# Kernel tuning notes

Measured on AMD Instinct MI355X. Metric: run time of the kernel, lower is better.

The kernel has to match this reference:

```python
import jax, jax.numpy as jnp
import numpy as np

D_MODEL = 2048; D_STATE = 64; D_CONV = 4; EXPAND = 2
N_HEADS = 64; N_GROUPS = 1; CHUNK = 256
D_INNER = D_MODEL * EXPAND            # 4096
HEAD_DIM = D_INNER // N_HEADS         # 64
XBC_DIM = D_INNER + 2 * N_GROUPS * D_STATE   # 4224
D_IN_PROJ = 2 * D_INNER + 2 * N_GROUPS * D_STATE + N_HEADS  # 8384
EPS = 1.1920929e-07  # torch.finfo(float32).eps (nn.RMSNorm default)


def setup_inputs() -> dict:
    key = jax.random.key(0)
    ks = jax.random.split(key, 4)
    x = jax.random.normal(ks[0], (2, 2048, D_MODEL), jnp.float32)
    in_proj_w = jax.random.normal(ks[1], (D_IN_PROJ, D_MODEL), jnp.float32) * (D_MODEL ** -0.5)
    conv_w = jax.random.normal(ks[2], (XBC_DIM, 1, D_CONV), jnp.float32) * (D_CONV ** -0.5)
    conv_b = jnp.zeros((XBC_DIM,), jnp.float32)
    rng = np.random.default_rng(0)
    dt = np.exp(rng.standard_normal(N_HEADS) * (np.log(0.1) - np.log(0.001)) + np.log(0.001))
    dt = np.clip(dt, 1e-4, None)
    dt_bias = jnp.asarray(dt + np.log(-np.expm1(-dt)), jnp.float32)
    A_log = jnp.asarray(np.log(rng.uniform(1.0, 16.0, N_HEADS)), jnp.float32)
    D_param = jnp.ones((N_HEADS,), jnp.float32)
    norm_w = jnp.ones((D_INNER,), jnp.float32)
    out_proj_w = jax.random.normal(ks[3], (D_MODEL, D_INNER), jnp.float32) * (D_INNER ** -0.5)
    return dict(x=x, in_proj_w=in_proj_w, conv_w=conv_w, conv_b=conv_b,
                dt_bias=dt_bias, A_log=A_log, D_param=D_param,
                norm_w=norm_w, out_proj_w=out_proj_w)


def segsum(a):
    # a: (..., T) -> lower-triangular segment sums, -inf above diagonal
    T = a.shape[-1]
    cs = jnp.cumsum(a, axis=-1)
    seg = cs[..., :, None] - cs[..., None, :]
    mask = jnp.tril(jnp.ones((T, T), dtype=bool))
    return jnp.where(mask, seg, -jnp.inf)


def ssd_minimal_discrete(X, A, B, C, block_len):
    # X: (b,l,h,p)  A: (b,l,h)  B,C: (b,l,h,n)
    b, l, h, p = X.shape
    c = l // block_len
    X = X.reshape(b, c, block_len, h, p)
    A = A.reshape(b, c, block_len, h).transpose(0, 3, 1, 2)  # b h c l
    B = B.reshape(b, c, block_len, h, -1)
    C = C.reshape(b, c, block_len, h, -1)
    A_cumsum = jnp.cumsum(A, axis=-1)
    # 1. intra-chunk (diagonal block) output
    L = jnp.exp(segsum(A))
    Y_diag = jnp.einsum('bclhn,bcshn,bhcls,bcshp->bclhp', C, B, L, X)
    # 2. per-chunk states
    decay_states = jnp.exp(A_cumsum[..., -1:] - A_cumsum)
    states = jnp.einsum('bclhn,bhcl,bclhp->bchpn', B, decay_states, X)
    # 3. inter-chunk recurrence (initial state = 0)
    states = jnp.concatenate([jnp.zeros_like(states[:, :1]), states], axis=1)
    decay_chunk = jnp.exp(segsum(jnp.pad(A_cumsum[..., -1], ((0, 0), (0, 0), (1, 0)))))
    new_states = jnp.einsum('bhzc,bchpn->bzhpn', decay_chunk, states)
    states_in, final_state = new_states[:, :-1], new_states[:, -1]
    # 4. state -> output conversion
    Y_off = jnp.einsum('bclhn,bchpn,bhcl->bclhp', C, states_in, jnp.exp(A_cumsum))
    return (Y_diag + Y_off).reshape(b, l, h, p), final_state


def reference(x, in_proj_w, conv_w, conv_b, dt_bias, A_log, D_param, norm_w, out_proj_w):
    b, L, _ = x.shape
    A = -jnp.exp(A_log)                                     # (h,)
    zxbcdt = x @ in_proj_w.T                                # (b,L,d_in_proj)
    z = zxbcdt[..., :D_INNER]
    xBC = zxbcdt[..., D_INNER:D_INNER + XBC_DIM]
    dt = jax.nn.softplus(zxbcdt[..., D_INNER + XBC_DIM:] + dt_bias)  # (b,L,h)
    # causal depthwise conv1d (padding=d_conv-1, then truncate to seqlen)
    xc = jax.lax.conv_general_dilated(
        xBC.transpose(0, 2, 1), conv_w, (1,), [(D_CONV - 1, 0)],
        dimension_numbers=('NCH', 'OIH', 'NCH'), feature_group_count=XBC_DIM)
    xBC = jax.nn.silu(xc + conv_b[None, :, None]).transpose(0, 2, 1)
    xs = xBC[..., :D_INNER].reshape(b, L, N_HEADS, HEAD_DIM)
    Bm = xBC[..., D_INNER:D_INNER + N_GROUPS * D_STATE].reshape(b, L, N_GROUPS, D_STATE)
    Cm = xBC[..., D_INNER + N_GROUPS * D_STATE:].reshape(b, L, N_GROUPS, D_STATE)
    rep = N_HEADS // N_GROUPS
    Bm = jnp.repeat(Bm, rep, axis=2)
    Cm = jnp.repeat(Cm, rep, axis=2)
    y, _ = ssd_minimal_discrete(xs * dt[..., None], A * dt, Bm, Cm, CHUNK)
    y = y + xs * D_param[None, None, :, None]
    y = y.reshape(b, L, D_INNER)
    y = z * jax.nn.silu(y)
    y = y * jax.lax.rsqrt(jnp.mean(y * y, axis=-1, keepdims=True) + EPS) * norm_w
    return y @ out_proj_w.T
```

## Files before the change

### kernel.cpp

```cpp
#include <hip/hip_runtime.h>
#include <math.h>

#define D_MODEL   2048
#define D_INNER   4096
#define XBC_DIM   4224
#define D_IN_PROJ 8384
#define N_ZX      8320
#define NH    64
#define HD    64
#define DS    64
#define LCH   256
#define NCH   8
#define LSEQ  2048
#define TTOK  4096
#define EPS_R 1.1920929e-07f

#define XT_S 264
#define WL_S 72
#define GEMM_IN_BLKS ((N_ZX / 128) * (TTOK / 128))

typedef unsigned short u16;
typedef unsigned int   u32;
typedef _Float16 f16x8 __attribute__((ext_vector_type(8)));
typedef _Float16 f16x4 __attribute__((ext_vector_type(4)));
typedef float    f4v   __attribute__((ext_vector_type(4)));

__device__ __forceinline__ float4 f16_ld4(const _Float16* c, size_t idx) {
    f16x4 v = *(const f16x4*)(c + idx);
    return make_float4((float)v[0], (float)v[1], (float)v[2], (float)v[3]);
}
__device__ __forceinline__ f16x8 cvt8(float4 a, float4 b) {
    f16x8 r;
    r[0] = (_Float16)a.x; r[1] = (_Float16)a.y; r[2] = (_Float16)a.z; r[3] = (_Float16)a.w;
    r[4] = (_Float16)b.x; r[5] = (_Float16)b.y; r[6] = (_Float16)b.z; r[7] = (_Float16)b.w;
    return r;
}
__device__ __forceinline__ float fexp(float x)  { return __expf(x); }
__device__ __forceinline__ float fsilu(float x) { return x / (1.f + __expf(-x)); }
__device__ __forceinline__ int xcd_swz(int orig, int nwg) {
    int cpx = nwg >> 3;
    return (orig & 7) * cpx + (orig >> 3);
}
__device__ __forceinline__ void gload16(const _Float16* g, _Float16* l) {
    __builtin_amdgcn_global_load_lds(
        (const __attribute__((address_space(1))) u32*)g,
        (__attribute__((address_space(3))) u32*)l, 16, 0, 0);
}

#define NX8  ((size_t)TTOK * D_MODEL / 8)
#define NW8  ((size_t)N_ZX * D_MODEL / 8)
#define NO8  ((size_t)D_MODEL * D_INNER / 8)
__global__ __launch_bounds__(256) void cvt_all_kernel(const float* __restrict__ x,
                                                      const float* __restrict__ w_in,
                                                      const float* __restrict__ w_out,
                                                      const float* __restrict__ nw,
                                                      _Float16* __restrict__ x16,
                                                      _Float16* __restrict__ win16,
                                                      _Float16* __restrict__ wout16) {
    size_t i = (size_t)blockIdx.x * 256 + threadIdx.x;
    if (i < NX8) {
        size_t base = i * 8;
        float4 a = *(const float4*)(x + base);
        float4 b = *(const float4*)(x + base + 4);
        *(f16x8*)(x16 + base) = cvt8(a, b);
    } else if (i < NX8 + NW8) {
        size_t base = (i - NX8) * 8;
        float4 a = *(const float4*)(w_in + base);
        float4 b = *(const float4*)(w_in + base + 4);
        *(f16x8*)(win16 + base) = cvt8(a, b);
    } else if (i < NX8 + NW8 + NO8) {
        size_t base = (i - NX8 - NW8) * 8;
        int k = (int)(base & 4095);
        float4 a = *(const float4*)(w_out + base);
        float4 b = *(const float4*)(w_out + base + 4);
        float4 na = *(const float4*)(nw + k);
        float4 nb = *(const float4*)(nw + k + 4);
        a.x *= na.x; a.y *= na.y; a.z *= na.z; a.w *= na.w;
        b.x *= nb.x; b.y *= nb.y; b.z *= nb.z; b.w *= nb.w;
        *(f16x8*)(wout16 + base) = cvt8(a, b);
    }
}

__global__ __launch_bounds__(256) void gemm_in_dt(const _Float16* __restrict__ A,
                                                  const _Float16* __restrict__ W,
                                                  _Float16* __restrict__ zf,
                                                  _Float16* __restrict__ cbuf,
                                                  const float* __restrict__ x,
                                                  const float* __restrict__ w_in,
                                                  const float* __restrict__ dt_bias,
                                                  float* __restrict__ dt_buf) {
    __shared__ __align__(16) char smem[65536];
    const int tid = threadIdx.x;

    if (blockIdx.x < 256) {
        float* Xs = (float*)smem;
        float* Ws = (float*)(smem + 4096);
        int t0 = blockIdx.x * 16;
        int h = tid & 63, trow = tid >> 6;
        float acc[4] = {0.f, 0.f, 0.f, 0.f};
        const float* wdt = w_in + (size_t)(D_INNER + XBC_DIM) * D_MODEL;

        for (int k0 = 0; k0 < D_MODEL; k0 += 64) {
            __syncthreads();
            {
                int r = tid >> 4, c4 = (tid & 15) * 4;
                *(float4*)&Xs[r * 64 + c4] =
                    *(const float4*)(x + (size_t)(t0 + r) * D_MODEL + k0 + c4);
            }
            #pragma unroll
            for (int i = 0; i < 4; ++i) {
                int ff = tid + i * 256;
                int r = ff >> 4, c4 = (ff & 15) * 4;
                float4 v = *(const float4*)(wdt + (size_t)r * D_MODEL + k0 + c4);
                Ws[r * 65 + c4 + 0] = v.x; Ws[r * 65 + c4 + 1] = v.y;
                Ws[r * 65 + c4 + 2] = v.z; Ws[r * 65 + c4 + 3] = v.w;
            }
            __syncthreads();
            #pragma unroll 16
            for (int k = 0; k < 64; ++k) {
                float wv = Ws[h * 65 + k];
                #pragma unroll
                for (int i = 0; i < 4; ++i)
                    acc[i] += Xs[(trow + i * 4) * 64 + k] * wv;
            }
        }
        float bias = dt_bias[h];
        #pragma unroll
        for (int i = 0; i < 4; ++i) {
            float xv = acc[i] + bias;
            float sp = (xv > 20.f) ? xv : log1pf(expf(xv));
            dt_buf[(size_t)(t0 + trow + i * 4) * 64 + h] = sp;
        }
        return;
    }

    _Float16* lsA = (_Float16*)smem;
    _Float16* lsB = (_Float16*)(smem + 32768);
    const int lane = tid & 63, w = tid >> 6;
    int swz = xcd_swz((int)blockIdx.x - 256, GEMM_IN_BLKS);
    const int row0 = (swz / (N_ZX / 128)) * 128, col0 = (swz % (N_ZX / 128)) * 128;
    const int wr = w >> 1, wc = w & 1;
    const int fr = lane & 15, fq = lane >> 4;

    auto stage = [&](int buf, int k0) {
        #pragma unroll
        for (int i = 0; i < 4; ++i) {
            int obase = i * 4096 + w * 1024;
            int o = obase + lane * 16;
            int row = o >> 7, b0 = o & 127;
            int lb = b0 ^ ((row & 7) << 4);
            gload16(A + (size_t)(row0 + row) * D_MODEL + k0 + (lb >> 1),
                    lsA + buf * 8192 + (obase >> 1));
            gload16(W + (size_t)(col0 + row) * D_MODEL + k0 + (lb >> 1),
                    lsB + buf * 8192 + (obase >> 1));
        }
    };

    f4v acc[4][4];
    #pragma unroll
    for (int mi = 0; mi < 4; ++mi)
        #pragma unroll
        for (int ni = 0; ni < 4; ++ni) acc[mi][ni] = (f4v){0.f, 0.f, 0.f, 0.f};

    stage(0, 0);
    __syncthreads();
    int cur = 0;
    for (int k0 = 0; k0 < D_MODEL; k0 += 64) {
        if (k0 + 64 < D_MODEL) stage(cur ^ 1, k0 + 64);
        f16x8 ah[4][2];
        #pragma unroll
        for (int mi = 0; mi < 4; ++mi)
            #pragma unroll
            for (int kf = 0; kf < 2; ++kf) {
                int r = wr * 64 + mi * 16 + fr;
                int pb = (kf * 64 + fq * 16) ^ ((r & 7) << 4);
                ah[mi][kf] = *(const f16x8*)((const char*)lsA + cur * 16384 + r * 128 + pb);
            }
        #pragma unroll
        for (int ni = 0; ni < 4; ++ni) {
            #pragma unroll
            for (int kf = 0; kf < 2; ++kf) {
                int rb = wc * 64 + ni * 16 + fr;
                int pb = (kf * 64 + fq * 16) ^ ((rb & 7) << 4);
                f16x8 bh = *(const f16x8*)((const char*)lsB + cur * 16384 + rb * 128 + pb);
                #pragma unroll
                for (int mi = 0; mi < 4; ++mi)
                    acc[mi][ni] = __builtin_amdgcn_mfma_f32_16x16x32_f16(ah[mi][kf], bh, acc[mi][ni], 0, 0, 0);
            }
        }
        __syncthreads();
        cur ^= 1;
    }

    const int orow = fq * 4;
    #pragma unroll
    for (int mi = 0; mi < 4; ++mi)
        #pragma unroll
        for (int ni = 0; ni < 4; ++ni) {
            int r = row0 + wr * 64 + mi * 16 + orow;
            int cc = col0 + wc * 64 + ni * 16 + fr;
            if (col0 < D_INNER) {
                #pragma unroll
                for (int j = 0; j < 4; ++j)
                    zf[(size_t)(r + j) * D_INNER + cc] = (_Float16)acc[mi][ni][j];
            } else {
                #pragma unroll
                for (int j = 0; j < 4; ++j)
                    cbuf[(size_t)(r + j) * XBC_DIM + (cc - D_INNER)] = (_Float16)acc[mi][ni][j];
            }
        }
}

__global__ __launch_bounds__(256) void scan_bc_kernel(const float* __restrict__ dt_buf,
                                                      const float* __restrict__ A_log,
                                                      float* __restrict__ acs,
                                                      const _Float16* __restrict__ cbuf,
                                                      const float* __restrict__ cw,
                                                      const float* __restrict__ cb,
                                                      _Float16* __restrict__ bc) {
    int tid = threadIdx.x;
    if (blockIdx.x < 1024) {
        int bh = blockIdx.x >> 3, c = blockIdx.x & 7;
        int b = bh >> 6, h = bh & 63;
        float Ah = -expf(A_log[h]);
        __shared__ float s[256];
        int t = b * LSEQ + c * LCH + tid;
        float a = Ah * dt_buf[t * 64 + h];
        s[tid] = a;
        __syncthreads();
        for (int off = 1; off < 256; off <<= 1) {
            float v = (tid >= off) ? s[tid - off] : 0.f;
            __syncthreads();
            s[tid] += v;
            __syncthreads();
        }
        acs[(size_t)bh * LSEQ + c * LCH + tid] = s[tid];
    } else {
        int t = ((int)blockIdx.x - 1024) * 2 + (tid >> 7);
        int chl = tid & 127;
        int b = t >> 11, lp = t & 2047;
        int ch = D_INNER + chl;
        float acc = cb[ch];
        #pragma unroll
        for (int j = 0; j < 4; ++j) {
            int lj = lp - 3 + j;
            if (lj >= 0)
                acc += cw[ch * 4 + j] * (float)cbuf[(size_t)(b * LSEQ + lj) * XBC_DIM + ch];
        }
        bc[(size_t)t * 128 + chl] = (_Float16)fsilu(acc);
    }
}

__global__ __launch_bounds__(256) void gemm_out16(const _Float16* __restrict__ A,
                                                  const _Float16* __restrict__ W,
                                                  float* __restrict__ C,
                                                  const float* __restrict__ usq) {
    __shared__ __align__(16) _Float16 lsA[2][128 * 64];
    __shared__ __align__(16) _Float16 lsB[2][128 * 64];
    __shared__ float rstd_l[128];
    const int tid = threadIdx.x, lane = tid & 63, w = tid >> 6;
    int swz = xcd_swz(blockIdx.x, (D_MODEL / 128) * (TTOK / 128));
    const int row0 = (swz / (D_MODEL / 128)) * 128, col0 = (swz % (D_MODEL / 128)) * 128;
    const int wr = w >> 1, wc = w & 1;
    const int fr = lane & 15, fq = lane >> 4;

    auto stage = [&](int buf, int k0) {
        #pragma unroll
        for (int i = 0; i < 4; ++i) {
            int obase = i * 4096 + w * 1024;
            int o = obase + lane * 16;
            int row = o >> 7, b0 = o & 127;
            int lb = b0 ^ ((row & 7) << 4);
            gload16(A + (size_t)(row0 + row) * D_INNER + k0 + (lb >> 1), &lsA[buf][obase >> 1]);
            gload16(W + (size_t)(col0 + row) * D_INNER + k0 + (lb >> 1), &lsB[buf][obase >> 1]);
        }
    };

    if (tid < 128) {
        const float* uq = usq + (size_t)(row0 + tid) * 64;
        float s = 0.f;
        #pragma unroll
        for (int i = 0; i < 16; ++i) {
            float4 v = *(const float4*)(uq + i * 4);
            s += v.x + v.y + v.z + v.w;
        }
        rstd_l[tid] = rsqrtf(s / 4096.f + EPS_R);
    }

    f4v acc[4][4];
    #pragma unroll
    for (int mi = 0; mi < 4; ++mi)
        #pragma unroll
        for (int ni = 0; ni < 4; ++ni) acc[mi][ni] = (f4v){0.f, 0.f, 0.f, 0.f};

    stage(0, 0);
    __syncthreads();
    int cur = 0;
    for (int k0 = 0; k0 < D_INNER; k0 += 64) {
        if (k0 + 64 < D_INNER) stage(cur ^ 1, k0 + 64);
        f16x8 ah[4][2];
        #pragma unroll
        for (int mi = 0; mi < 4; ++mi)
            #pragma unroll
            for (int kf = 0; kf < 2; ++kf) {
                int r = wr * 64 + mi * 16 + fr;
                int pb = (kf * 64 + fq * 16) ^ ((r & 7) << 4);
                ah[mi][kf] = *(const f16x8*)((const char*)&lsA[cur][0] + r * 128 + pb);
            }
        #pragma unroll
        for (int ni = 0; ni < 4; ++ni) {
            #pragma unroll
            for (int kf = 0; kf < 2; ++kf) {
                int rb = wc * 64 + ni * 16 + fr;
                int pb = (kf * 64 + fq * 16) ^ ((rb & 7) << 4);
                f16x8 bh = *(const f16x8*)((const char*)&lsB[cur][0] + rb * 128 + pb);
                #pragma unroll
                for (int mi = 0; mi < 4; ++mi)
                    acc[mi][ni] = __builtin_amdgcn_mfma_f32_16x16x32_f16(ah[mi][kf], bh, acc[mi][ni], 0, 0, 0);
            }
        }
        __syncthreads();
        cur ^= 1;
    }

    const int orow = fq * 4;
    #pragma unroll
    for (int mi = 0; mi < 4; ++mi)
        #pragma unroll
        for (int ni = 0; ni < 4; ++ni) {
            int rl = wr * 64 + mi * 16 + orow;
            int cc = col0 + wc * 64 + ni * 16 + fr;
            #pragma unroll
            for (int j = 0; j < 4; ++j)
                C[(size_t)(row0 + rl + j) * D_MODEL + cc] = acc[mi][ni][j] * rstd_l[rl + j];
        }
}

__global__ __launch_bounds__(256) void chunkstate_mfma(const _Float16* __restrict__ cbuf,
                                                       const _Float16* __restrict__ bc,
                                                       const float* __restrict__ cw,
                                                       const float* __restrict__ cb,
                                                       const float* __restrict__ dt_buf,
                                                       const float* __restrict__ acs,
                                                       float* __restrict__ states,
                                                       _Float16* __restrict__ xts) {
    const int h = blockIdx.x & 63;
    const int c = (blockIdx.x >> 6) & 7;
    const int b = blockIdx.x >> 9;
    const int tbase = b * LSEQ + c * LCH;
    const int tid = threadIdx.x, lane = tid & 63, w = tid >> 6;
    const int fr = lane & 15, fq = lane >> 4;

    __shared__ __align__(16) _Float16 XT[64][XT_S];
    __shared__ __align__(16) _Float16 BT[64][XT_S];
    __shared__ float acs_s[256], dts[256], wdec[256];

    const float* acs_blk = acs + (size_t)(b * 64 + h) * LSEQ + c * LCH;
    acs_s[tid] = acs_blk[tid];
    dts[tid] = dt_buf[(size_t)(tbase + tid) * 64 + h];
    __syncthreads();
    const float acs_last = acs_s[LCH - 1];
    wdec[tid] = fexp(acs_last - acs_s[tid]) * dts[tid];

    #pragma unroll 4
    for (int i = 0; i < 16; ++i) {
        int u = tid + i * 256;
        int s = u >> 4, pq = (u & 15) * 4;
        int lp = c * LCH + s;
        int ch0 = h * HD + pq;
        float tp[4][4];
        #pragma unroll
        for (int k = 0; k < 4; ++k)
            *(float4*)tp[k] = *(const float4*)(cw + (size_t)(ch0 + k) * 4);
        float a0 = cb[ch0], a1 = cb[ch0 + 1], a2 = cb[ch0 + 2], a3 = cb[ch0 + 3];
        #pragma unroll
        for (int j = 0; j < 4; ++j) {
            int lj = lp - 3 + j;
            if (lj >= 0) {
                float4 v = f16_ld4(cbuf, (size_t)(b * LSEQ + lj) * XBC_DIM + ch0);
                a0 += tp[0][j] * v.x; a1 += tp[1][j] * v.y;
                a2 += tp[2][j] * v.z; a3 += tp[3][j] * v.w;
            }
        }
        XT[pq + 0][s] = (_Float16)fsilu(a0);
        XT[pq + 1][s] = (_Float16)fsilu(a1);
        XT[pq + 2][s] = (_Float16)fsilu(a2);
        XT[pq + 3][s] = (_Float16)fsilu(a3);
    }
    __syncthreads();
    #pragma unroll 4
    for (int i = 0; i < 16; ++i) {
        int u = tid + i * 256;
        int s = u >> 4, n4 = (u & 15) * 4;
        f16x4 v = *(const f16x4*)(bc + (size_t)(tbase + s) * 128 + n4);
        float wd = wdec[s];
        BT[n4 + 0][s] = (_Float16)((float)v[0] * wd);
        BT[n4 + 1][s] = (_Float16)((float)v[1] * wd);
        BT[n4 + 2][s] = (_Float16)((float)v[2] * wd);
        BT[n4 + 3][s] = (_Float16)((float)v[3] * wd);
    }
    __syncthreads();

    f4v acc[4];
    #pragma unroll
    for (int nf = 0; nf < 4; ++nf) acc[nf] = (f4v){0.f, 0.f, 0.f, 0.f};
    __builtin_amdgcn_s_setprio(1);
    #pragma unroll
    for (int ks = 0; ks < 8; ++ks) {
        f16x8 af = *(const f16x8*)&XT[w * 16 + fr][ks * 32 + fq * 8];
        #pragma unroll
        for (int nf = 0; nf < 4; ++nf) {
            f16x8 bf = *(const f16x8*)&BT[nf * 16 + fr][ks * 32 + fq * 8];
            acc[nf] = __builtin_amdgcn_mfma_f32_16x16x32_f16(af, bf, acc[nf], 0, 0, 0);
        }
    }
    __builtin_amdgcn_s_setprio(0);
    float* sp = states + (size_t)blockIdx.x * 4096;
    #pragma unroll
    for (int nf = 0; nf < 4; ++nf)
        #pragma unroll
        for (int r = 0; r < 4; ++r)
            sp[(size_t)(w * 16 + fq * 4 + r) * 64 + nf * 16 + fr] = acc[nf][r];

    {
        _Float16* xd = xts + (size_t)blockIdx.x * 16384 + tid * 64;
        int pp = tid >> 2, s0 = (tid & 3) * 64;
        #pragma unroll
        for (int i = 0; i < 8; ++i)
            *(f16x8*)(xd + i * 8) = *(const f16x8*)&XT[pp][s0 + i * 8];
    }
}

__global__ __launch_bounds__(256) void chunkscan_kernel(const float* __restrict__ acs,
                                                        float* __restrict__ states) {
    int b = blockIdx.x >> 6, h = blockIdx.x & 63;
    int tid = threadIdx.x;
    float4 S4[4];
    #pragma unroll
    for (int i = 0; i < 4; ++i) S4[i] = make_float4(0.f, 0.f, 0.f, 0.f);
    const float* acs_blk = acs + (size_t)blockIdx.x * LSEQ;
    for (int c = 0; c < NCH; ++c) {
        float d = expf(acs_blk[c * LCH + LCH - 1]);
        float4* sp = (float4*)(states + ((size_t)(b * NCH + c) * NH + h) * 4096 + tid * 16);
        float4 t4[4];
        #pragma unroll
        for (int i = 0; i < 4; ++i) t4[i] = sp[i];
        #pragma unroll
        for (int i = 0; i < 4; ++i) sp[i] = S4[i];
        #pragma unroll
        for (int i = 0; i < 4; ++i) {
            S4[i].x = d * S4[i].x + t4[i].x;
            S4[i].y = d * S4[i].y + t4[i].y;
            S4[i].z = d * S4[i].z + t4[i].z;
            S4[i].w = d * S4[i].w + t4[i].w;
        }
    }
}

__global__ __launch_bounds__(256) void ymerged_mfma(const _Float16* __restrict__ xts,
                                                    const _Float16* __restrict__ bc,
                                                    _Float16* __restrict__ zf,
                                                    const float* __restrict__ dt_buf,
                                                    const float* __restrict__ acs,
                                                    const float* __restrict__ states,
                                                    const float* __restrict__ D_param,
                                                    float* __restrict__ usq) {
    const int h = blockIdx.x & 63;
    const int c = (blockIdx.x >> 6) & 7;
    const int b = blockIdx.x >> 9;
    const int tbase = b * LSEQ + c * LCH;
    const int tid = threadIdx.x, lane = tid & 63, w = tid >> 6;
    const int fr = lane & 15, fq = lane >> 4;

    __shared__ __align__(16) _Float16 XT[64][XT_S];
    __shared__ __align__(16) _Float16 Wl[4][64][WL_S];
    __shared__ float acs_s[256];
    __shared__ float dts[256];

    const float* acs_blk = acs + (size_t)(b * 64 + h) * LSEQ + c * LCH;
    acs_s[tid] = acs_blk[tid];
    dts[tid] = dt_buf[(size_t)(tbase + tid) * 64 + h];

    {
        const _Float16* xs = xts + (size_t)blockIdx.x * 16384 + tid * 64;
        int pp = tid >> 2, s0 = (tid & 3) * 64;
        #pragma unroll
        for (int i = 0; i < 8; ++i)
            *(f16x8*)&XT[pp][s0 + i * 8] = *(const f16x8*)(xs + i * 8);
    }
    __syncthreads();

    f16x8 cf[4][2];
    #pragma unroll
    for (int ls = 0; ls < 4; ++ls)
        #pragma unroll
        for (int kf = 0; kf < 2; ++kf)
            cf[ls][kf] = *(const f16x8*)(bc + (size_t)(tbase + w * 64 + ls * 16 + fr) * 128
                                         + 64 + kf * 32 + fq * 8);

    float acsl[16];
    #pragma unroll
    for (int ls = 0; ls < 4; ++ls)
        #pragma unroll
        for (int r = 0; r < 4; ++r)
            acsl[ls * 4 + r] = acs_s[w * 64 + ls * 16 + fq * 4 + r];

    f4v Y[4][4];
    {
        f16x8 sf[4][2];
        #pragma unroll
        for (int ps = 0; ps < 4; ++ps)
            #pragma unroll
            for (int kf = 0; kf < 2; ++kf) {
                const float* src = states + (size_t)blockIdx.x * 4096
                                 + (ps * 16 + fr) * 64 + kf * 32 + fq * 8;
                sf[ps][kf] = cvt8(*(const float4*)src, *(const float4*)(src + 4));
            }
        f4v yo[4][4];
        __builtin_amdgcn_s_setprio(1);
        #pragma unroll
        for (int ls = 0; ls < 4; ++ls)
            #pragma unroll
            for (int ps = 0; ps < 4; ++ps) {
                yo[ls][ps] = (f4v){0.f, 0.f, 0.f, 0.f};
                yo[ls][ps] = __builtin_amdgcn_mfma_f32_16x16x32_f16(cf[ls][0], sf[ps][0], yo[ls][ps], 0, 0, 0);
                yo[ls][ps] = __builtin_amdgcn_mfma_f32_16x16x32_f16(cf[ls][1], sf[ps][1], yo[ls][ps], 0, 0, 0);
            }
        __builtin_amdgcn_s_setprio(0);
        #pragma unroll
        for (int ls = 0; ls < 4; ++ls)
            #pragma unroll
            for (int ps = 0; ps < 4; ++ps)
                #pragma unroll
                for (int r = 0; r < 4; ++r)
                    Y[ls][ps][r] = fexp(acsl[ls * 4 + r]) * yo[ls][ps][r];
    }

    for (int st = 0; st <= w; ++st) {
        f16x8 bf[4][2];
        #pragma unroll
        for (int ss = 0; ss < 4; ++ss)
            #pragma unroll
            for (int kf = 0; kf < 2; ++kf)
                bf[ss][kf] = *(const f16x8*)(bc + (size_t)(tbase + st * 64 + ss * 16 + fr) * 128
                                             + kf * 32 + fq * 8);
        f4v S[4][4];
        __builtin_amdgcn_s_setprio(1);
        #pragma unroll
        for (int ls = 0; ls < 4; ++ls)
            #pragma unroll
            for (int ss = 0; ss < 4; ++ss) {
                S[ls][ss] = (f4v){0.f, 0.f, 0.f, 0.f};
                S[ls][ss] = __builtin_amdgcn_mfma_f32_16x16x32_f16(cf[ls][0], bf[ss][0], S[ls][ss], 0, 0, 0);
                S[ls][ss] = __builtin_amdgcn_mfma_f32_16x16x32_f16(cf[ls][1], bf[ss][1], S[ls][ss], 0, 0, 0);
            }
        __builtin_amdgcn_s_setprio(0);
        #pragma unroll
        for (int ss = 0; ss < 4; ++ss) {
            int s_idx = st * 64 + ss * 16 + fr;
            float as = acs_s[s_idx];
            float dv = dts[s_idx];
            #pragma unroll
            for (int ls = 0; ls < 4; ++ls)
                #pragma unroll
                for (int r = 0; r < 4; ++r) {
                    int l_idx = w * 64 + ls * 16 + fq * 4 + r;
                    float wv = (s_idx <= l_idx)
                             ? fexp(acsl[ls * 4 + r] - as) * dv * S[ls][ss][r] : 0.f;
                    Wl[w][ls * 16 + fq * 4 + r][ss * 16 + fr] = (_Float16)wv;
                }
        }
        f16x8 wf[4][2], xf[4][2];
        #pragma unroll
        for (int ls = 0; ls < 4; ++ls)
            #pragma unroll
            for (int kf = 0; kf < 2; ++kf)
                wf[ls][kf] = *(const f16x8*)&Wl[w][ls * 16 + fr][kf * 32 + fq * 8];
        #pragma unroll
        for (int ps = 0; ps < 4; ++ps)
            #pragma unroll
            for (int kf = 0; kf < 2; ++kf)
                xf[ps][kf] = *(const f16x8*)&XT[ps * 16 + fr][st * 64 + kf * 32 + fq * 8];
        __builtin_amdgcn_s_setprio(1);
        #pragma unroll
        for (int ls = 0; ls < 4; ++ls)
            #pragma unroll
            for (int ps = 0; ps < 4; ++ps) {
                Y[ls][ps] = __builtin_amdgcn_mfma_f32_16x16x32_f16(wf[ls][0], xf[ps][0], Y[ls][ps], 0, 0, 0);
                Y[ls][ps] = __builtin_amdgcn_mfma_f32_16x16x32_f16(wf[ls][1], xf[ps][1], Y[ls][ps], 0, 0, 0);
            }
        __builtin_amdgcn_s_setprio(0);
    }

    float Dp = D_param[h];
    #pragma unroll
    for (int ls = 0; ls < 4; ++ls)
        #pragma unroll
        for (int r = 0; r < 4; ++r) {
            int ll = ls * 16 + fq * 4 + r;
            int l = w * 64 + ll;
            int tl = tbase + l;
            #pragma unroll
            for (int ps = 0; ps < 4; ++ps) {
                int p = ps * 16 + fr;
                float y = Y[ls][ps][r] + (float)XT[p][l] * Dp;
                float uv = (float)zf[(size_t)tl * D_INNER + h * HD + p] * fsilu(y);
                Wl[w][ll][p] = (_Float16)uv;
            }
        }
    {
        int l = w * 64 + lane;
        int tl = tbase + l;
        _Float16* dst = zf + (size_t)tl * D_INNER + h * HD;
        float ss = 0.f;
        #pragma unroll
        for (int i = 0; i < 8; ++i) {
            f16x8 v = *(const f16x8*)&Wl[w][lane][i * 8];
            *(f16x8*)(dst + i * 8) = v;
            #pragma unroll
            for (int j = 0; j < 8; ++j) { float f = (float)v[j]; ss += f * f; }
        }
        usq[(size_t)tl * 64 + h] = ss;
    }
}

extern "C" void kernel_launch(void* const* d_in, const int* in_sizes, int n_in,
                              void* d_out, int out_size, void* d_ws, size_t ws_size,
                              hipStream_t stream) {
    const float* x        = (const float*)d_in[0];
    const float* w_in     = (const float*)d_in[1];
    const float* conv_w   = (const float*)d_in[2];
    const float* conv_b   = (const float*)d_in[3];
    const float* dt_bias  = (const float*)d_in[4];
    const float* A_log    = (const float*)d_in[5];
    const float* D_param  = (const float*)d_in[6];
    const float* norm_w   = (const float*)d_in[7];
    const float* w_out    = (const float*)d_in[8];
    float* out = (float*)d_out;

    const size_t sz_zf  = (size_t)TTOK * D_INNER * 2;
    const size_t sz_cb  = (size_t)TTOK * XBC_DIM * 2;
    const size_t sz_x16 = (size_t)TTOK * D_MODEL * 2;
    const size_t sz_wi  = (size_t)N_ZX * D_MODEL * 2;
    const size_t sz_wo  = (size_t)D_MODEL * D_INNER * 2;
    const size_t sz_bc  = (size_t)TTOK * 128 * 2;
    const size_t sz_dt  = (size_t)TTOK * 64 * 4;
    const size_t sz_acs = (size_t)128 * LSEQ * 4;
    const size_t sz_st  = (size_t)1024 * 4096 * 4;
    const size_t need = sz_zf + sz_cb + sz_x16 + sz_wi + sz_wo
                      + sz_bc + sz_dt + sz_acs + sz_st;
    if (ws_size < need) return;

    char* p = (char*)d_ws;
    _Float16* zf     = (_Float16*)p; p += sz_zf;
    _Float16* cbuf   = (_Float16*)p; p += sz_cb;
    _Float16* x16    = (_Float16*)p; p += sz_x16;
    _Float16* win16  = (_Float16*)p; p += sz_wi;
    _Float16* wout16 = (_Float16*)p; p += sz_wo;
    _Float16* bc     = (_Float16*)p; p += sz_bc;
    float*    dtb    = (float*)p;    p += sz_dt;
    float*    acs    = (float*)p;    p += sz_acs;
    float*    states = (float*)p;    p += sz_st;
    float* usq = dtb;
    _Float16* xts = (_Float16*)d_out;

    {
        size_t total8 = NX8 + NW8 + NO8;
        cvt_all_kernel<<<(u32)((total8 + 255) / 256), 256, 0, stream>>>(
            x, w_in, w_out, norm_w, x16, win16, wout16);
    }
    gemm_in_dt<<<256 + GEMM_IN_BLKS, 256, 0, stream>>>(
        x16, win16, zf, cbuf, x, w_in, dt_bias, dtb);
    scan_bc_kernel<<<1024 + 2048, 256, 0, stream>>>(
        dtb, A_log, acs, cbuf, conv_w, conv_b, bc);
    chunkstate_mfma<<<2 * NCH * NH, 256, 0, stream>>>(
        cbuf, bc, conv_w, conv_b, dtb, acs, states, xts);
    chunkscan_kernel<<<2 * NH, 256, 0, stream>>>(acs, states);
    ymerged_mfma<<<2 * NCH * NH, 256, 0, stream>>>(
        xts, bc, zf, dtb, acs, states, D_param, usq);
    gemm_out16<<<(D_MODEL / 128) * (TTOK / 128), 256, 0, stream>>>(zf, wout16, out, usq);
}
```

Baseline: 469.0 us.

## Fuse A-cumsum and B/C conv into chunkstate kernel; band-swizzle GEMM tile order

Removes the separate scan_bc kernel. Each chunkstate block now computes its own per-chunk cumsum of A*dt and recomputes the causal conv plus SiLU for the B channels inline. Blocks with h==0 and h==1 also write the B and C conv outputs to bc for the later ymerged kernel. Both GEMMs also remap tiles so that groups of four row-tiles share a column sweep, which should improve L2 reuse. The aim is to save a launch and a global round trip, at the cost of redundant B-conv work in every block and some imbalance on the h==1 blocks.

New measurement: 475.3 us. Within noise of the previous version (+1.3%).

```diff
diff --git a/kernel.cpp b/kernel.cpp
--- a/kernel.cpp
+++ b/kernel.cpp
@@ -138,7 +138,9 @@
     _Float16* lsB = (_Float16*)(smem + 32768);
     const int lane = tid & 63, w = tid >> 6;
     int swz = xcd_swz((int)blockIdx.x - 256, GEMM_IN_BLKS);
-    const int row0 = (swz / (N_ZX / 128)) * 128, col0 = (swz % (N_ZX / 128)) * 128;
+    int band = swz / 260, idx = swz % 260;
+    const int row0 = (band * 4 + (idx & 3)) * 128;
+    const int col0 = (idx >> 2) * 128;
     const int wr = w >> 1, wc = w & 1;
     const int fr = lane & 15, fq = lane >> 4;
 
@@ -211,46 +213,6 @@
         }
 }
 
-__global__ __launch_bounds__(256) void scan_bc_kernel(const float* __restrict__ dt_buf,
-                                                      const float* __restrict__ A_log,
-                                                      float* __restrict__ acs,
-                                                      const _Float16* __restrict__ cbuf,
-                                                      const float* __restrict__ cw,
-                                                      const float* __restrict__ cb,
-                                                      _Float16* __restrict__ bc) {
-    int tid = threadIdx.x;
-    if (blockIdx.x < 1024) {
-        int bh = blockIdx.x >> 3, c = blockIdx.x & 7;
-        int b = bh >> 6, h = bh & 63;
-        float Ah = -expf(A_log[h]);
-        __shared__ float s[256];
-        int t = b * LSEQ + c * LCH + tid;
-        float a = Ah * dt_buf[t * 64 + h];
-        s[tid] = a;
-        __syncthreads();
-        for (int off = 1; off < 256; off <<= 1) {
-            float v = (tid >= off) ? s[tid - off] : 0.f;
-            __syncthreads();
-            s[tid] += v;
-            __syncthreads();
-        }
-        acs[(size_t)bh * LSEQ + c * LCH + tid] = s[tid];
-    } else {
-        int t = ((int)blockIdx.x - 1024) * 2 + (tid >> 7);
-        int chl = tid & 127;
-        int b = t >> 11, lp = t & 2047;
-        int ch = D_INNER + chl;
-        float acc = cb[ch];
-        #pragma unroll
-        for (int j = 0; j < 4; ++j) {
-            int lj = lp - 3 + j;
-            if (lj >= 0)
-                acc += cw[ch * 4 + j] * (float)cbuf[(size_t)(b * LSEQ + lj) * XBC_DIM + ch];
-        }
-        bc[(size_t)t * 128 + chl] = (_Float16)fsilu(acc);
-    }
-}
-
 __global__ __launch_bounds__(256) void gemm_out16(const _Float16* __restrict__ A,
                                                   const _Float16* __restrict__ W,
                                                   float* __restrict__ C,
@@ -260,7 +222,9 @@
     __shared__ float rstd_l[128];
     const int tid = threadIdx.x, lane = tid & 63, w = tid >> 6;
     int swz = xcd_swz(blockIdx.x, (D_MODEL / 128) * (TTOK / 128));
-    const int row0 = (swz / (D_MODEL / 128)) * 128, col0 = (swz % (D_MODEL / 128)) * 128;
+    int band = swz / 64, idx = swz % 64;
+    const int row0 = (band * 4 + (idx & 3)) * 128;
+    const int col0 = (idx >> 2) * 128;
     const int wr = w >> 1, wc = w & 1;
     const int fr = lane & 15, fq = lane >> 4;
 
@@ -337,13 +301,14 @@
 }
 
 __global__ __launch_bounds__(256) void chunkstate_mfma(const _Float16* __restrict__ cbuf,
-                                                       const _Float16* __restrict__ bc,
                                                        const float* __restrict__ cw,
                                                        const float* __restrict__ cb,
                                                        const float* __restrict__ dt_buf,
-                                                       const float* __restrict__ acs,
+                                                       const float* __restrict__ A_log,
+                                                       float* __restrict__ acs,
                                                        float* __restrict__ states,
-                                                       _Float16* __restrict__ xts) {
+                                                       _Float16* __restrict__ xts,
+                                                       _Float16* __restrict__ bc) {
     const int h = blockIdx.x & 63;
     const int c = (blockIdx.x >> 6) & 7;
     const int b = blockIdx.x >> 9;
@@ -355,12 +320,20 @@
     __shared__ __align__(16) _Float16 BT[64][XT_S];
     __shared__ float acs_s[256], dts[256], wdec[256];
 
-    const float* acs_blk = acs + (size_t)(b * 64 + h) * LSEQ + c * LCH;
-    acs_s[tid] = acs_blk[tid];
+    float Ah = -expf(A_log[h]);
     dts[tid] = dt_buf[(size_t)(tbase + tid) * 64 + h];
+    acs_s[tid] = Ah * dts[tid];
     __syncthreads();
+    for (int off = 1; off < 256; off <<= 1) {
+        float v = (tid >= off) ? acs_s[tid - off] : 0.f;
+        __syncthreads();
+        acs_s[tid] += v;
+        __syncthreads();
+    }
+    acs[(size_t)(b * 64 + h) * LSEQ + c * LCH + tid] = acs_s[tid];
     const float acs_last = acs_s[LCH - 1];
     wdec[tid] = fexp(acs_last - acs_s[tid]) * dts[tid];
+    __syncthreads();
 
     #pragma unroll 4
     for (int i = 0; i < 16; ++i) {
@@ -387,17 +360,63 @@
         XT[pq + 2][s] = (_Float16)fsilu(a2);
         XT[pq + 3][s] = (_Float16)fsilu(a3);
     }
-    __syncthreads();
     #pragma unroll 4
     for (int i = 0; i < 16; ++i) {
         int u = tid + i * 256;
         int s = u >> 4, n4 = (u & 15) * 4;
-        f16x4 v = *(const f16x4*)(bc + (size_t)(tbase + s) * 128 + n4);
+        int lp = c * LCH + s;
+        int ch0 = D_INNER + n4;
+        float tp[4][4];
+        #pragma unroll
+        for (int k = 0; k < 4; ++k)
+            *(float4*)tp[k] = *(const float4*)(cw + (size_t)(ch0 + k) * 4);
+        float a0 = cb[ch0], a1 = cb[ch0 + 1], a2 = cb[ch0 + 2], a3 = cb[ch0 + 3];
+        #pragma unroll
+        for (int j = 0; j < 4; ++j) {
+            int lj = lp - 3 + j;
+            if (lj >= 0) {
+                float4 v = f16_ld4(cbuf, (size_t)(b * LSEQ + lj) * XBC_DIM + ch0);
+                a0 += tp[0][j] * v.x; a1 += tp[1][j] * v.y;
+                a2 += tp[2][j] * v.z; a3 += tp[3][j] * v.w;
+            }
+        }
+        float s0 = fsilu(a0), s1 = fsilu(a1), s2 = fsilu(a2), s3 = fsilu(a3);
         float wd = wdec[s];
-        BT[n4 + 0][s] = (_Float16)((float)v[0] * wd);
-        BT[n4 + 1][s] = (_Float16)((float)v[1] * wd);
-        BT[n4 + 2][s] = (_Float16)((float)v[2] * wd);
-        BT[n4 + 3][s] = (_Float16)((float)v[3] * wd);
+        BT[n4 + 0][s] = (_Float16)(s0 * wd);
+        BT[n4 + 1][s] = (_Float16)(s1 * wd);
+        BT[n4 + 2][s] = (_Float16)(s2 * wd);
+        BT[n4 + 3][s] = (_Float16)(s3 * wd);
+        if (h == 0) {
+            _Float16* br = bc + (size_t)(tbase + s) * 128 + n4;
+            br[0] = (_Float16)s0; br[1] = (_Float16)s1;
+            br[2] = (_Float16)s2; br[3] = (_Float16)s3;
+        }
+    }
+    if (h == 1) {
+        #pragma unroll 4
+        for (int i = 0; i < 16; ++i) {
+            int u = tid + i * 256;
+            int s = u >> 4, n4 = (u & 15) * 4 + 64;
+            int lp = c * LCH + s;
+            int ch0 = D_INNER + n4;
+            float tp[4][4];
+            #pragma unroll
+            for (int k = 0; k < 4; ++k)
+                *(float4*)tp[k] = *(const float4*)(cw + (size_t)(ch0 + k) * 4);
+            float a0 = cb[ch0], a1 = cb[ch0 + 1], a2 = cb[ch0 + 2], a3 = cb[ch0 + 3];
+            #pragma unroll
+            for (int j = 0; j < 4; ++j) {
+                int lj = lp - 3 + j;
+                if (lj >= 0) {
+                    float4 v = f16_ld4(cbuf, (size_t)(b * LSEQ + lj) * XBC_DIM + ch0);
+                    a0 += tp[0][j] * v.x; a1 += tp[1][j] * v.y;
+                    a2 += tp[2][j] * v.z; a3 += tp[3][j] * v.w;
+                }
+            }
+            _Float16* br = bc + (size_t)(tbase + s) * 128 + n4;
+            br[0] = (_Float16)fsilu(a0); br[1] = (_Float16)fsilu(a1);
+            br[2] = (_Float16)fsilu(a2); br[3] = (_Float16)fsilu(a3);
+        }
     }
     __syncthreads();
 
@@ -671,10 +690,8 @@
     }
     gemm_in_dt<<<256 + GEMM_IN_BLKS, 256, 0, stream>>>(
         x16, win16, zf, cbuf, x, w_in, dt_bias, dtb);
-    scan_bc_kernel<<<1024 + 2048, 256, 0, stream>>>(
-        dtb, A_log, acs, cbuf, conv_w, conv_b, bc);
     chunkstate_mfma<<<2 * NCH * NH, 256, 0, stream>>>(
-        cbuf, bc, conv_w, conv_b, dtb, acs, states, xts);
+        cbuf, conv_w, conv_b, dtb, A_log, acs, states, xts, bc);
     chunkscan_kernel<<<2 * NH, 256, 0, stream>>>(acs, states);
     ymerged_mfma<<<2 * NCH * NH, 256, 0, stream>>>(
         xts, bc, zf, dtb, acs, states, D_param, usq);
```
